# Kernel tuning notes

Hardware: AMD Instinct MI355X
Metric: run time of the kernel (lower is better)

The kernel has to match this reference:

```python
import jax, jax.numpy as jnp
import numpy as np

DIM = 1024
HIDDEN = 2816  # multiple_of * ceil(int(2*4096/3)/multiple_of)
N_MODALITIES = 2
B, S = 8, 4096


def setup_inputs() -> dict:
    key = jax.random.key(0)
    k_x, k_m, k1, k2, k3 = jax.random.split(key, 5)
    x = jax.random.normal(k_x, (B, S, DIM), dtype=jnp.float32)
    modality_ids = jax.random.randint(k_m, (B, S), 0, N_MODALITIES, dtype=jnp.int32)
    in_std = DIM ** -0.5
    out_std = HIDDEN ** -0.5
    # Linear weight layout: [out_features, in_features], stacked over modalities.
    W1 = jax.random.normal(k1, (N_MODALITIES, HIDDEN, DIM), dtype=jnp.float32) * in_std
    W3 = jax.random.normal(k3, (N_MODALITIES, HIDDEN, DIM), dtype=jnp.float32) * in_std
    W2 = jax.random.normal(k2, (N_MODALITIES, DIM, HIDDEN), dtype=jnp.float32) * out_std
    return {"x": x, "modality_ids": modality_ids, "W1": W1, "W2": W2, "W3": W3}


def reference(x, modality_ids, W1, W2, W3):
    # Masked per-modality SwiGLU; equivalent to gather -> expert MLP -> scatter.
    output = jnp.zeros_like(x)
    for m in range(N_MODALITIES):  # small fixed modality count
        mask = (modality_ids == m)[..., None]          # [B, S, 1]
        x1 = jnp.einsum('bsd,hd->bsh', x, W1[m])       # gate proj
        x3 = jnp.einsum('bsd,hd->bsh', x, W3[m])       # up proj
        out_m = jnp.einsum('bsh,dh->bsd', jax.nn.silu(x1) * x3, W2[m])
        output = output + jnp.where(mask, out_m, 0.0)
    return output
```

## Files before the change

kernel.cpp:

```cpp
#include <hip/hip_runtime.h>
#include <stdint.h>

#define DIMK 1024
#define HID  2816

typedef __attribute__((ext_vector_type(8))) __bf16 bf16x8;
typedef __attribute__((ext_vector_type(4))) float  f32x4;

typedef const __attribute__((address_space(1))) void* gas1_t;
typedef __attribute__((address_space(3))) void*       las3_t;

__device__ __forceinline__ uint16_t f2bf(float f) {
  uint32_t u = __float_as_uint(f);
  u += 0x7FFFu + ((u >> 16) & 1u);
  return (uint16_t)(u >> 16);
}

__device__ __forceinline__ void gload16(const uint16_t* g, uint16_t* l) {
  __builtin_amdgcn_global_load_lds((gas1_t)g, (las3_t)l, 16, 0, 0);
}

template<int N> __device__ __forceinline__ void wait_vm() {
  if constexpr (N == 0)      asm volatile("s_waitcnt vmcnt(0)" ::: "memory");
  else if constexpr (N == 2) asm volatile("s_waitcnt vmcnt(2)" ::: "memory");
  else                       asm volatile("s_waitcnt vmcnt(6)" ::: "memory");
}

__device__ __forceinline__ void stage_half(const uint16_t* g, long stride,
                                           uint16_t* lds, int wv, int lane) {
  const int rsub = lane >> 3;
  const int gsw  = ((lane & 7) ^ rsub) << 3;
#pragma unroll
  for (int j = 0; j < 2; ++j) {
    const int blk = j * 8 + wv;
    gload16(g + (long)(blk * 8 + rsub) * stride + gsw,
            lds + blk * 512 + lane * 8);
  }
}

__device__ __forceinline__ bf16x8 ldsf(const uint16_t* lds, int r, int g) {
  return *reinterpret_cast<const bf16x8*>(lds + r * 64 + ((g ^ (r & 7)) << 3));
}


__global__ void count_kernel(const int* __restrict__ mids, int* __restrict__ bc, int T) {
  const int b = blockIdx.x, t = threadIdx.x;
  const int token = b * 256 + t;
  const int lane = t & 63, wv = t >> 6;
  const int m = (token < T) ? mids[token] : -1;
  unsigned long long m0 = __ballot(m == 0);
  unsigned long long m1 = __ballot(m == 1);
  __shared__ int w0[4], w1[4];
  if (lane == 0) { w0[wv] = __popcll(m0); w1[wv] = __popcll(m1); }
  __syncthreads();
  if (t == 0) {
    bc[2 * b]     = w0[0] + w0[1] + w0[2] + w0[3];
    bc[2 * b + 1] = w1[0] + w1[1] + w1[2] + w1[3];
  }
}

__global__ void scan_kernel(const int* __restrict__ bc, int* __restrict__ base,
                            int* __restrict__ counters, int nb) {
  __shared__ int s0[256], s1[256];
  const int t = threadIdx.x;
  const int v0 = (t < nb) ? bc[2 * t] : 0;
  const int v1 = (t < nb) ? bc[2 * t + 1] : 0;
  s0[t] = v0; s1[t] = v1;
  __syncthreads();
  for (int off = 1; off < 256; off <<= 1) {
    int a0 = (t >= off) ? s0[t - off] : 0;
    int a1 = (t >= off) ? s1[t - off] : 0;
    __syncthreads();
    s0[t] += a0; s1[t] += a1;
    __syncthreads();
  }
  if (t < nb) { base[2 * t] = s0[t] - v0; base[2 * t + 1] = s1[t] - v1; }
  if (t == nb - 1) { counters[0] = s0[t]; counters[1] = s1[t]; }
}

__global__ void slot_kernel(const int* __restrict__ mids, const int* __restrict__ base,
                            const int* __restrict__ counters, int* __restrict__ tok,
                            int* __restrict__ slotof, int T) {
  const int b = blockIdx.x, t = threadIdx.x;
  const int token = b * 256 + t;
  const int lane = t & 63, wv = t >> 6;
  const int m = (token < T) ? mids[token] : -1;
  unsigned long long m0 = __ballot(m == 0);
  unsigned long long m1 = __ballot(m == 1);
  __shared__ int w0[4], w1[4];
  if (lane == 0) { w0[wv] = __popcll(m0); w1[wv] = __popcll(m1); }
  __syncthreads();
  int pre0 = 0, pre1 = 0;
  for (int w = 0; w < wv; ++w) { pre0 += w0[w]; pre1 += w1[w]; }
  if (token >= T) return;
  const unsigned long long below = (1ULL << lane) - 1ULL;
  const int c0 = counters[0];
  const int al0 = ((c0 + 255) >> 8) << 8;
  int slot;
  if (m == 0) slot = base[2 * b] + pre0 + __popcll(m0 & below);
  else        slot = al0 + base[2 * b + 1] + pre1 + __popcll(m1 & below);
  tok[slot] = token;
  slotof[token] = slot;
}

__global__ void copy_kernel(const float* __restrict__ x, const int* __restrict__ slotof,
                            uint16_t* __restrict__ xg, int T) {
  const int token = blockIdx.x * 4 + (threadIdx.x >> 6);
  if (token >= T) return;
  const int lane = threadIdx.x & 63;
  const int slot = slotof[token];
  const float4* src = (const float4*)(x + (long)token * DIMK);
  uint16_t* dst = xg + (long)slot * DIMK;
#pragma unroll
  for (int j = 0; j < 4; ++j) {
    float4 v = src[lane + 64 * j];
    ushort4 o;
    o.x = f2bf(v.x); o.y = f2bf(v.y); o.z = f2bf(v.z); o.w = f2bf(v.w);
    *(ushort4*)(dst + (lane + 64 * j) * 4) = o;
  }
}

__global__ void convert_kernel(const float* __restrict__ src, uint16_t* __restrict__ dst, long n) {
  long i = ((long)blockIdx.x * blockDim.x + threadIdx.x) * 4;
  if (i >= n) return;
  float4 v = *(const float4*)(src + i);
  ushort4 o;
  o.x = f2bf(v.x); o.y = f2bf(v.y); o.z = f2bf(v.z); o.w = f2bf(v.w);
  *(ushort4*)(dst + i) = o;
}


template<bool PF, int W0, int W2>
__device__ __forceinline__ void g1_tile(
    const uint16_t* Ac, const uint16_t* B1c, const uint16_t* B3c,
    uint16_t* An, uint16_t* B1n, uint16_t* B3n,
    const uint16_t* gA, const uint16_t* gB1, const uint16_t* gB3, long ko,
    int wv, int lane, int wr, int wc, int lrow, int grp,
    f32x4 (&accG)[8][2], f32x4 (&accU)[8][2]) {
  bf16x8 a[4][2], b1[2][2], b3[2][2];
  wait_vm<W0>();
  __builtin_amdgcn_s_barrier();
  asm volatile("" ::: "memory");
#pragma unroll
  for (int m = 0; m < 4; ++m)
    a[m][0] = ldsf(Ac, m * 32 + wr * 16 + lrow, grp);
#pragma unroll
  for (int n = 0; n < 2; ++n) {
    b1[n][0] = ldsf(B1c, wc * 32 + n * 16 + lrow, grp);
    b3[n][0] = ldsf(B3c, wc * 32 + n * 16 + lrow, grp);
  }
  if constexpr (PF) {
    stage_half(gA  + ko, DIMK, An,  wv, lane);
    stage_half(gB1 + ko, DIMK, B1n, wv, lane);
    stage_half(gB3 + ko, DIMK, B3n, wv, lane);
  }
  asm volatile("s_waitcnt lgkmcnt(0)" ::: "memory");
  __builtin_amdgcn_sched_barrier(0);
  __builtin_amdgcn_s_setprio(1);
#pragma unroll
  for (int m = 0; m < 4; ++m)
#pragma unroll
    for (int n = 0; n < 2; ++n) {
      accG[m][n] = __builtin_amdgcn_mfma_f32_16x16x32_bf16(a[m][0], b1[n][0], accG[m][n], 0, 0, 0);
      accU[m][n] = __builtin_amdgcn_mfma_f32_16x16x32_bf16(a[m][0], b3[n][0], accU[m][n], 0, 0, 0);
    }
  __builtin_amdgcn_s_setprio(0);
#pragma unroll
  for (int m = 0; m < 4; ++m)
    a[m][1] = ldsf(Ac, m * 32 + wr * 16 + lrow, 4 + grp);
#pragma unroll
  for (int n = 0; n < 2; ++n) {
    b1[n][1] = ldsf(B1c, wc * 32 + n * 16 + lrow, 4 + grp);
    b3[n][1] = ldsf(B3c, wc * 32 + n * 16 + lrow, 4 + grp);
  }
  asm volatile("s_waitcnt lgkmcnt(0)" ::: "memory");
  __builtin_amdgcn_sched_barrier(0);
  __builtin_amdgcn_s_setprio(1);
#pragma unroll
  for (int m = 0; m < 4; ++m)
#pragma unroll
    for (int n = 0; n < 2; ++n) {
      accG[m][n] = __builtin_amdgcn_mfma_f32_16x16x32_bf16(a[m][1], b1[n][1], accG[m][n], 0, 0, 0);
      accU[m][n] = __builtin_amdgcn_mfma_f32_16x16x32_bf16(a[m][1], b3[n][1], accU[m][n], 0, 0, 0);
    }
  __builtin_amdgcn_s_setprio(0);
  wait_vm<W2>();
  __builtin_amdgcn_s_barrier();
  asm volatile("" ::: "memory");
#pragma unroll
  for (int m = 0; m < 4; ++m)
    a[m][0] = ldsf(Ac, (m + 4) * 32 + wr * 16 + lrow, grp);
  if constexpr (PF) stage_half(gA + 128 * DIMK + ko, DIMK, An + 128 * 64, wv, lane);
  asm volatile("s_waitcnt lgkmcnt(0)" ::: "memory");
  __builtin_amdgcn_sched_barrier(0);
  __builtin_amdgcn_s_setprio(1);
#pragma unroll
  for (int m = 0; m < 4; ++m)
#pragma unroll
    for (int n = 0; n < 2; ++n) {
      accG[m + 4][n] = __builtin_amdgcn_mfma_f32_16x16x32_bf16(a[m][0], b1[n][0], accG[m + 4][n], 0, 0, 0);
      accU[m + 4][n] = __builtin_amdgcn_mfma_f32_16x16x32_bf16(a[m][0], b3[n][0], accU[m + 4][n], 0, 0, 0);
    }
  __builtin_amdgcn_s_setprio(0);
#pragma unroll
  for (int m = 0; m < 4; ++m)
    a[m][1] = ldsf(Ac, (m + 4) * 32 + wr * 16 + lrow, 4 + grp);
  asm volatile("s_waitcnt lgkmcnt(0)" ::: "memory");
  __builtin_amdgcn_sched_barrier(0);
  __builtin_amdgcn_s_setprio(1);
#pragma unroll
  for (int m = 0; m < 4; ++m)
#pragma unroll
    for (int n = 0; n < 2; ++n) {
      accG[m + 4][n] = __builtin_amdgcn_mfma_f32_16x16x32_bf16(a[m][1], b1[n][1], accG[m + 4][n], 0, 0, 0);
      accU[m + 4][n] = __builtin_amdgcn_mfma_f32_16x16x32_bf16(a[m][1], b3[n][1], accU[m + 4][n], 0, 0, 0);
    }
  __builtin_amdgcn_s_setprio(0);
}

__global__ __launch_bounds__(512, 2) void gemm1_kernel(
    const uint16_t* __restrict__ xg, const uint16_t* __restrict__ w1b,
    const uint16_t* __restrict__ w3b, uint16_t* __restrict__ hbuf,
    const int* __restrict__ counters) {
  __shared__ __align__(16) uint16_t lsA[2][256 * 64];
  __shared__ __align__(16) uint16_t lsB1[2][128 * 64];
  __shared__ __align__(16) uint16_t lsB3[2][128 * 64];

  const int c0 = counters[0], c1 = counters[1];
  const int t0 = (c0 + 255) >> 8, t1 = (c1 + 255) >> 8;
  const int NHT = gridDim.y;
  const int nwg = gridDim.x * NHT;
  const int orig = blockIdx.y * gridDim.x + blockIdx.x;
  const int q = nwg >> 3, r = nwg & 7;
  const int xcd = orig & 7, loc = orig >> 3;
  const int swz = (xcd < r ? xcd * (q + 1) : r * (q + 1) + (xcd - r) * q) + loc;
  const int rt = swz / NHT;
  const int ht = swz - rt * NHT;
  if (rt >= t0 + t1) return;
  const int mod = (rt < t0) ? 0 : 1;
  const long row0 = (long)rt * 256;

  const int tid = threadIdx.x, lane = tid & 63, wv = tid >> 6;
  const int wr = wv >> 2, wc = wv & 3;
  const int lrow = lane & 15, grp = lane >> 4;

  const uint16_t* gA  = xg  + row0 * DIMK;
  const uint16_t* gB1 = w1b + ((long)mod * HID + ht * 128) * DIMK;
  const uint16_t* gB3 = w3b + ((long)mod * HID + ht * 128) * DIMK;

  f32x4 accG[8][2], accU[8][2];
#pragma unroll
  for (int m = 0; m < 8; ++m)
#pragma unroll
    for (int n = 0; n < 2; ++n) {
      accG[m][n] = {0.f, 0.f, 0.f, 0.f};
      accU[m][n] = {0.f, 0.f, 0.f, 0.f};
    }

  stage_half(gA,              DIMK, &lsA[0][0],        wv, lane);
  stage_half(gB1,             DIMK, &lsB1[0][0],       wv, lane);
  stage_half(gB3,             DIMK, &lsB3[0][0],       wv, lane);
  stage_half(gA + 128 * DIMK, DIMK, &lsA[0][128 * 64], wv, lane);

  const int NT = DIMK / 64;
  int cur = 0;
  for (int t = 0; t < NT - 1; ++t) {
    g1_tile<true, 2, 6>(&lsA[cur][0], &lsB1[cur][0], &lsB3[cur][0],
                        &lsA[cur ^ 1][0], &lsB1[cur ^ 1][0], &lsB3[cur ^ 1][0],
                        gA, gB1, gB3, (long)(t + 1) * 64,
                        wv, lane, wr, wc, lrow, grp, accG, accU);
    cur ^= 1;
  }
  g1_tile<false, 2, 0>(&lsA[cur][0], &lsB1[cur][0], &lsB3[cur][0],
                       &lsA[cur ^ 1][0], &lsB1[cur ^ 1][0], &lsB3[cur ^ 1][0],
                       gA, gB1, gB3, 0,
                       wv, lane, wr, wc, lrow, grp, accG, accU);

#pragma unroll
  for (int m = 0; m < 8; ++m)
#pragma unroll
    for (int n = 0; n < 2; ++n) {
      const int col = ht * 128 + wc * 32 + n * 16 + lrow;
#pragma unroll
      for (int i = 0; i < 4; ++i) {
        const long row = row0 + m * 32 + wr * 16 + grp * 4 + i;
        float g = accG[m][n][i];
        float u = accU[m][n][i];
        float hv = (g / (1.f + __expf(-g))) * u;
        hbuf[row * HID + col] = f2bf(hv);
      }
    }
}


template<bool PF, int W0, int W2>
__device__ __forceinline__ void g2_tile(
    const uint16_t* Ac, const uint16_t* Bc, uint16_t* An, uint16_t* Bn,
    const uint16_t* gA, const uint16_t* gB, long ko,
    int wv, int lane, int wr, int wc, int lrow, int grp,
    f32x4 (&acc)[8][4]) {
  bf16x8 a[4][2], b[4][2];
  wait_vm<W0>();
  __builtin_amdgcn_s_barrier();
  asm volatile("" ::: "memory");
#pragma unroll
  for (int m = 0; m < 4; ++m)
    a[m][0] = ldsf(Ac, m * 32 + wr * 16 + lrow, grp);
#pragma unroll
  for (int n = 0; n < 4; ++n)
    b[n][0] = ldsf(Bc, wc * 64 + n * 16 + lrow, grp);
  if constexpr (PF) {
    stage_half(gA + ko,             HID, An,            wv, lane);
    stage_half(gB + ko,             HID, Bn,            wv, lane);
    stage_half(gB + 128 * HID + ko, HID, Bn + 128 * 64, wv, lane);
  }
  asm volatile("s_waitcnt lgkmcnt(0)" ::: "memory");
  __builtin_amdgcn_sched_barrier(0);
  __builtin_amdgcn_s_setprio(1);
#pragma unroll
  for (int m = 0; m < 4; ++m)
#pragma unroll
    for (int n = 0; n < 4; ++n)
      acc[m][n] = __builtin_amdgcn_mfma_f32_16x16x32_bf16(a[m][0], b[n][0], acc[m][n], 0, 0, 0);
  __builtin_amdgcn_s_setprio(0);
#pragma unroll
  for (int m = 0; m < 4; ++m)
    a[m][1] = ldsf(Ac, m * 32 + wr * 16 + lrow, 4 + grp);
#pragma unroll
  for (int n = 0; n < 4; ++n)
    b[n][1] = ldsf(Bc, wc * 64 + n * 16 + lrow, 4 + grp);
  asm volatile("s_waitcnt lgkmcnt(0)" ::: "memory");
  __builtin_amdgcn_sched_barrier(0);
  __builtin_amdgcn_s_setprio(1);
#pragma unroll
  for (int m = 0; m < 4; ++m)
#pragma unroll
    for (int n = 0; n < 4; ++n)
      acc[m][n] = __builtin_amdgcn_mfma_f32_16x16x32_bf16(a[m][1], b[n][1], acc[m][n], 0, 0, 0);
  __builtin_amdgcn_s_setprio(0);
  wait_vm<W2>();
  __builtin_amdgcn_s_barrier();
  asm volatile("" ::: "memory");
#pragma unroll
  for (int m = 0; m < 4; ++m)
    a[m][0] = ldsf(Ac, (m + 4) * 32 + wr * 16 + lrow, grp);
  if constexpr (PF) stage_half(gA + 128 * HID + ko, HID, An + 128 * 64, wv, lane);
  asm volatile("s_waitcnt lgkmcnt(0)" ::: "memory");
  __builtin_amdgcn_sched_barrier(0);
  __builtin_amdgcn_s_setprio(1);
#pragma unroll
  for (int m = 0; m < 4; ++m)
#pragma unroll
    for (int n = 0; n < 4; ++n)
      acc[m + 4][n] = __builtin_amdgcn_mfma_f32_16x16x32_bf16(a[m][0], b[n][0], acc[m + 4][n], 0, 0, 0);
  __builtin_amdgcn_s_setprio(0);
#pragma unroll
  for (int m = 0; m < 4; ++m)
    a[m][1] = ldsf(Ac, (m + 4) * 32 + wr * 16 + lrow, 4 + grp);
  asm volatile("s_waitcnt lgkmcnt(0)" ::: "memory");
  __builtin_amdgcn_sched_barrier(0);
  __builtin_amdgcn_s_setprio(1);
#pragma unroll
  for (int m = 0; m < 4; ++m)
#pragma unroll
    for (int n = 0; n < 4; ++n)
      acc[m + 4][n] = __builtin_amdgcn_mfma_f32_16x16x32_bf16(a[m][1], b[n][1], acc[m + 4][n], 0, 0, 0);
  __builtin_amdgcn_s_setprio(0);
}

__global__ __launch_bounds__(512, 2) void gemm2_kernel(
    const uint16_t* __restrict__ hbuf, const uint16_t* __restrict__ w2b,
    const int* __restrict__ counters, const int* __restrict__ tok,
    float* __restrict__ out) {
  __shared__ __align__(16) uint16_t lsA[2][256 * 64];
  __shared__ __align__(16) uint16_t lsB[2][256 * 64];

  const int c0 = counters[0], c1 = counters[1];
  const int t0 = (c0 + 255) >> 8, t1 = (c1 + 255) >> 8;
  const int NCT = gridDim.y;
  const int nwg = gridDim.x * NCT;
  const int orig = blockIdx.y * gridDim.x + blockIdx.x;
  const int q = nwg >> 3, r = nwg & 7;
  const int xcd = orig & 7, loc = orig >> 3;
  const int swz = (xcd < r ? xcd * (q + 1) : r * (q + 1) + (xcd - r) * q) + loc;
  const int rt = swz / NCT;
  const int ct = swz - rt * NCT;
  if (rt >= t0 + t1) return;
  const int mod = (rt < t0) ? 0 : 1;
  const long row0 = (long)rt * 256;
  const int vlimit = (mod == 0) ? c0 : t0 * 256 + c1;

  const int tid = threadIdx.x, lane = tid & 63, wv = tid >> 6;
  const int wr = wv >> 2, wc = wv & 3;
  const int lrow = lane & 15, grp = lane >> 4;

  const uint16_t* gA = hbuf + row0 * HID;
  const uint16_t* gB = w2b + ((long)mod * DIMK + ct * 256) * HID;

  f32x4 acc[8][4];
#pragma unroll
  for (int m = 0; m < 8; ++m)
#pragma unroll
    for (int n = 0; n < 4; ++n) acc[m][n] = {0.f, 0.f, 0.f, 0.f};

  stage_half(gA,             HID, &lsA[0][0],        wv, lane);
  stage_half(gB,             HID, &lsB[0][0],        wv, lane);
  stage_half(gB + 128 * HID, HID, &lsB[0][128 * 64], wv, lane);
  stage_half(gA + 128 * HID, HID, &lsA[0][128 * 64], wv, lane);

  const int NT = HID / 64;
  int cur = 0;
  for (int t = 0; t < NT - 1; ++t) {
    g2_tile<true, 2, 6>(&lsA[cur][0], &lsB[cur][0],
                        &lsA[cur ^ 1][0], &lsB[cur ^ 1][0],
                        gA, gB, (long)(t + 1) * 64,
                        wv, lane, wr, wc, lrow, grp, acc);
    cur ^= 1;
  }
  g2_tile<false, 2, 0>(&lsA[cur][0], &lsB[cur][0],
                       &lsA[cur ^ 1][0], &lsB[cur ^ 1][0],
                       gA, gB, 0,
                       wv, lane, wr, wc, lrow, grp, acc);

#pragma unroll
  for (int m = 0; m < 8; ++m)
#pragma unroll
    for (int n = 0; n < 4; ++n) {
      const int col = ct * 256 + wc * 64 + n * 16 + lrow;
#pragma unroll
      for (int i = 0; i < 4; ++i) {
        const int row = (int)row0 + m * 32 + wr * 16 + grp * 4 + i;
        if (row < vlimit) {
          out[(long)tok[row] * DIMK + col] = acc[m][n][i];
        }
      }
    }
}

extern "C" void kernel_launch(void* const* d_in, const int* in_sizes, int n_in,
                              void* d_out, int out_size, void* d_ws, size_t ws_size,
                              hipStream_t stream) {
  const float* x    = (const float*)d_in[0];
  const int*   mids = (const int*)d_in[1];
  const float* W1   = (const float*)d_in[2];
  const float* W2   = (const float*)d_in[3];
  const float* W3   = (const float*)d_in[4];
  float* out = (float*)d_out;

  const int T   = in_sizes[1];
  const int NB  = (T + 255) / 256;
  const int CAP = ((T + 255) & ~255) + 256;

  char* ws = (char*)d_ws;
  int* counters = (int*)ws;
  int* bc   = (int*)(ws + 256);
  int* base = (int*)(ws + 256 + 2048);
  int* tok  = (int*)(ws + 256 + 4096);
  int* slotof = tok + ((CAP + 63) & ~63);
  size_t off = 256 + 4096 + (size_t)((CAP + 63) & ~63) * 4 + (size_t)((T + 63) & ~63) * 4;
  off = (off + 255) & ~(size_t)255;
  uint16_t* xg  = (uint16_t*)(ws + off); off += (size_t)CAP * DIMK * 2;
  uint16_t* w1b = (uint16_t*)(ws + off); off += (size_t)2 * HID * DIMK * 2;
  uint16_t* w3b = (uint16_t*)(ws + off); off += (size_t)2 * HID * DIMK * 2;
  uint16_t* w2b = (uint16_t*)(ws + off); off += (size_t)2 * DIMK * HID * 2;
  uint16_t* hbuf = (uint16_t*)(ws + off); off += (size_t)CAP * HID * 2;
  (void)ws_size; (void)n_in; (void)out_size;

  count_kernel<<<NB, 256, 0, stream>>>(mids, bc, T);
  scan_kernel<<<1, 256, 0, stream>>>(bc, base, counters, NB);
  slot_kernel<<<NB, 256, 0, stream>>>(mids, base, counters, tok, slotof, T);
  copy_kernel<<<(T + 3) / 4, 256, 0, stream>>>(x, slotof, xg, T);

  const long NW = (long)2 * HID * DIMK;
  const int cblk = (int)((NW / 4 + 255) / 256);
  convert_kernel<<<cblk, 256, 0, stream>>>(W1, w1b, NW);
  convert_kernel<<<cblk, 256, 0, stream>>>(W3, w3b, NW);
  convert_kernel<<<cblk, 256, 0, stream>>>(W2, w2b, NW);

  const int rtiles = CAP / 256;
  gemm1_kernel<<<dim3(rtiles, HID / 128), 512, 0, stream>>>(xg, w1b, w3b, hbuf, counters);
  gemm2_kernel<<<dim3(rtiles, DIMK / 256), 512, 0, stream>>>(hbuf, w2b, counters, tok, out);
}
```

Before: 767.2 us.

## Restructure GEMM main loops into 8-phase ping-pong schedule with barrier-separated MFMA clusters

Both GEMM kernels are rewritten around a two-k-tile iteration with eight phases. Each phase issues one LDS fragment load batch and one global-to-LDS stage, then runs a 16-MFMA cluster between explicit barriers with raised priority, in the style of a ping-pong schedule. Launch bounds drop from 2 to 1 workgroup per CU, so the two waves per SIMD interleave under explicit barriers instead of relying on occupancy. This adds many barriers and a finer vmcnt/lgkmcnt wait discipline, and risks stalls or hazards if the wait counts are off.

```diff
diff --git a/kernel.cpp b/kernel.cpp
--- a/kernel.cpp
+++ b/kernel.cpp
@@ -22,8 +22,18 @@
 
 template<int N> __device__ __forceinline__ void wait_vm() {
   if constexpr (N == 0)      asm volatile("s_waitcnt vmcnt(0)" ::: "memory");
-  else if constexpr (N == 2) asm volatile("s_waitcnt vmcnt(2)" ::: "memory");
-  else                       asm volatile("s_waitcnt vmcnt(6)" ::: "memory");
+  else if constexpr (N == 6) asm volatile("s_waitcnt vmcnt(6)" ::: "memory");
+}
+
+__device__ __forceinline__ void ph_sync() {
+  __builtin_amdgcn_s_barrier();
+  asm volatile("s_waitcnt lgkmcnt(0)" ::: "memory");
+  __builtin_amdgcn_sched_barrier(0);
+  __builtin_amdgcn_s_setprio(1);
+}
+__device__ __forceinline__ void ph_end() {
+  __builtin_amdgcn_s_setprio(0);
+  __builtin_amdgcn_s_barrier();
 }
 
 __device__ __forceinline__ void stage_half(const uint16_t* g, long stride,
@@ -40,6 +50,30 @@
 
 __device__ __forceinline__ bf16x8 ldsf(const uint16_t* lds, int r, int g) {
   return *reinterpret_cast<const bf16x8*>(lds + r * 64 + ((g ^ (r & 7)) << 3));
+}
+
+template<int MO>
+__device__ __forceinline__ void mfma16_g1(f32x4 (&acc)[8][2], const bf16x8 (&af)[4][2],
+                                          const bf16x8 (&bf)[2][2]) {
+#pragma unroll
+  for (int ks = 0; ks < 2; ++ks)
+#pragma unroll
+    for (int m = 0; m < 4; ++m)
+#pragma unroll
+      for (int n = 0; n < 2; ++n)
+        acc[m + MO][n] = __builtin_amdgcn_mfma_f32_16x16x32_bf16(af[m][ks], bf[n][ks], acc[m + MO][n], 0, 0, 0);
+}
+
+template<int MO, int NO>
+__device__ __forceinline__ void mfma16_g2(f32x4 (&acc)[8][4], const bf16x8 (&af)[4][2],
+                                          const bf16x8 (&bf)[4][2]) {
+#pragma unroll
+  for (int ks = 0; ks < 2; ++ks)
+#pragma unroll
+    for (int m = 0; m < 4; ++m)
+#pragma unroll
+      for (int n = 0; n < 2; ++n)
+        acc[m + MO][n + NO] = __builtin_amdgcn_mfma_f32_16x16x32_bf16(af[m][ks], bf[n + NO][ks], acc[m + MO][n + NO], 0, 0, 0);
 }
 
 
@@ -130,95 +164,95 @@
 }
 
 
-template<bool PF, int W0, int W2>
-__device__ __forceinline__ void g1_tile(
-    const uint16_t* Ac, const uint16_t* B1c, const uint16_t* B3c,
-    uint16_t* An, uint16_t* B1n, uint16_t* B3n,
-    const uint16_t* gA, const uint16_t* gB1, const uint16_t* gB3, long ko,
+template<bool LAST>
+__device__ __forceinline__ void g1_iter(
+    uint16_t* A0, uint16_t* B10, uint16_t* B30,
+    uint16_t* A1, uint16_t* B11, uint16_t* B31,
+    const uint16_t* gA, const uint16_t* gB1, const uint16_t* gB3,
+    long ko1, long ko2, long ko3,
     int wv, int lane, int wr, int wc, int lrow, int grp,
     f32x4 (&accG)[8][2], f32x4 (&accU)[8][2]) {
   bf16x8 a[4][2], b1[2][2], b3[2][2];
-  wait_vm<W0>();
-  __builtin_amdgcn_s_barrier();
-  asm volatile("" ::: "memory");
-#pragma unroll
-  for (int m = 0; m < 4; ++m)
-    a[m][0] = ldsf(Ac, m * 32 + wr * 16 + lrow, grp);
+
+#pragma unroll
+  for (int m = 0; m < 4; ++m) {
+    a[m][0] = ldsf(A0, m * 32 + wr * 16 + lrow, grp);
+    a[m][1] = ldsf(A0, m * 32 + wr * 16 + lrow, 4 + grp);
+  }
 #pragma unroll
   for (int n = 0; n < 2; ++n) {
-    b1[n][0] = ldsf(B1c, wc * 32 + n * 16 + lrow, grp);
-    b3[n][0] = ldsf(B3c, wc * 32 + n * 16 + lrow, grp);
-  }
-  if constexpr (PF) {
-    stage_half(gA  + ko, DIMK, An,  wv, lane);
-    stage_half(gB1 + ko, DIMK, B1n, wv, lane);
-    stage_half(gB3 + ko, DIMK, B3n, wv, lane);
-  }
-  asm volatile("s_waitcnt lgkmcnt(0)" ::: "memory");
-  __builtin_amdgcn_sched_barrier(0);
-  __builtin_amdgcn_s_setprio(1);
-#pragma unroll
-  for (int m = 0; m < 4; ++m)
-#pragma unroll
-    for (int n = 0; n < 2; ++n) {
-      accG[m][n] = __builtin_amdgcn_mfma_f32_16x16x32_bf16(a[m][0], b1[n][0], accG[m][n], 0, 0, 0);
-      accU[m][n] = __builtin_amdgcn_mfma_f32_16x16x32_bf16(a[m][0], b3[n][0], accU[m][n], 0, 0, 0);
-    }
-  __builtin_amdgcn_s_setprio(0);
-#pragma unroll
-  for (int m = 0; m < 4; ++m)
-    a[m][1] = ldsf(Ac, m * 32 + wr * 16 + lrow, 4 + grp);
+    b1[n][0] = ldsf(B10, wc * 32 + n * 16 + lrow, grp);
+    b1[n][1] = ldsf(B10, wc * 32 + n * 16 + lrow, 4 + grp);
+  }
+  stage_half(gA + 128 * DIMK + ko1, DIMK, A1 + 128 * 64, wv, lane);
+  asm volatile("s_waitcnt lgkmcnt(8)" ::: "memory");
+  ph_sync();
+  mfma16_g1<0>(accG, a, b1);
+  ph_end();
 #pragma unroll
   for (int n = 0; n < 2; ++n) {
-    b1[n][1] = ldsf(B1c, wc * 32 + n * 16 + lrow, 4 + grp);
-    b3[n][1] = ldsf(B3c, wc * 32 + n * 16 + lrow, 4 + grp);
-  }
-  asm volatile("s_waitcnt lgkmcnt(0)" ::: "memory");
-  __builtin_amdgcn_sched_barrier(0);
-  __builtin_amdgcn_s_setprio(1);
-#pragma unroll
-  for (int m = 0; m < 4; ++m)
-#pragma unroll
-    for (int n = 0; n < 2; ++n) {
-      accG[m][n] = __builtin_amdgcn_mfma_f32_16x16x32_bf16(a[m][1], b1[n][1], accG[m][n], 0, 0, 0);
-      accU[m][n] = __builtin_amdgcn_mfma_f32_16x16x32_bf16(a[m][1], b3[n][1], accU[m][n], 0, 0, 0);
-    }
-  __builtin_amdgcn_s_setprio(0);
-  wait_vm<W2>();
-  __builtin_amdgcn_s_barrier();
-  asm volatile("" ::: "memory");
-#pragma unroll
-  for (int m = 0; m < 4; ++m)
-    a[m][0] = ldsf(Ac, (m + 4) * 32 + wr * 16 + lrow, grp);
-  if constexpr (PF) stage_half(gA + 128 * DIMK + ko, DIMK, An + 128 * 64, wv, lane);
-  asm volatile("s_waitcnt lgkmcnt(0)" ::: "memory");
-  __builtin_amdgcn_sched_barrier(0);
-  __builtin_amdgcn_s_setprio(1);
-#pragma unroll
-  for (int m = 0; m < 4; ++m)
-#pragma unroll
-    for (int n = 0; n < 2; ++n) {
-      accG[m + 4][n] = __builtin_amdgcn_mfma_f32_16x16x32_bf16(a[m][0], b1[n][0], accG[m + 4][n], 0, 0, 0);
-      accU[m + 4][n] = __builtin_amdgcn_mfma_f32_16x16x32_bf16(a[m][0], b3[n][0], accU[m + 4][n], 0, 0, 0);
-    }
-  __builtin_amdgcn_s_setprio(0);
-#pragma unroll
-  for (int m = 0; m < 4; ++m)
-    a[m][1] = ldsf(Ac, (m + 4) * 32 + wr * 16 + lrow, 4 + grp);
-  asm volatile("s_waitcnt lgkmcnt(0)" ::: "memory");
-  __builtin_amdgcn_sched_barrier(0);
-  __builtin_amdgcn_s_setprio(1);
-#pragma unroll
-  for (int m = 0; m < 4; ++m)
-#pragma unroll
-    for (int n = 0; n < 2; ++n) {
-      accG[m + 4][n] = __builtin_amdgcn_mfma_f32_16x16x32_bf16(a[m][1], b1[n][1], accG[m + 4][n], 0, 0, 0);
-      accU[m + 4][n] = __builtin_amdgcn_mfma_f32_16x16x32_bf16(a[m][1], b3[n][1], accU[m + 4][n], 0, 0, 0);
-    }
-  __builtin_amdgcn_s_setprio(0);
-}
-
-__global__ __launch_bounds__(512, 2) void gemm1_kernel(
+    b3[n][0] = ldsf(B30, wc * 32 + n * 16 + lrow, grp);
+    b3[n][1] = ldsf(B30, wc * 32 + n * 16 + lrow, 4 + grp);
+  }
+  if constexpr (!LAST) stage_half(gA + ko2, DIMK, A0, wv, lane);
+  ph_sync();
+  mfma16_g1<0>(accU, a, b3);
+  ph_end();
+#pragma unroll
+  for (int m = 0; m < 4; ++m) {
+    a[m][0] = ldsf(A0, (m + 4) * 32 + wr * 16 + lrow, grp);
+    a[m][1] = ldsf(A0, (m + 4) * 32 + wr * 16 + lrow, 4 + grp);
+  }
+  if constexpr (!LAST) stage_half(gB1 + ko2, DIMK, B10, wv, lane);
+  ph_sync();
+  mfma16_g1<4>(accG, a, b1);
+  ph_end();
+  if constexpr (!LAST) { stage_half(gB3 + ko2, DIMK, B30, wv, lane); wait_vm<6>(); }
+  else                 wait_vm<0>();
+  ph_sync();
+  mfma16_g1<4>(accU, a, b3);
+  ph_end();
+
+#pragma unroll
+  for (int m = 0; m < 4; ++m) {
+    a[m][0] = ldsf(A1, m * 32 + wr * 16 + lrow, grp);
+    a[m][1] = ldsf(A1, m * 32 + wr * 16 + lrow, 4 + grp);
+  }
+#pragma unroll
+  for (int n = 0; n < 2; ++n) {
+    b1[n][0] = ldsf(B11, wc * 32 + n * 16 + lrow, grp);
+    b1[n][1] = ldsf(B11, wc * 32 + n * 16 + lrow, 4 + grp);
+  }
+  if constexpr (!LAST) stage_half(gA + 128 * DIMK + ko2, DIMK, A0 + 128 * 64, wv, lane);
+  asm volatile("s_waitcnt lgkmcnt(8)" ::: "memory");
+  ph_sync();
+  mfma16_g1<0>(accG, a, b1);
+  ph_end();
+#pragma unroll
+  for (int n = 0; n < 2; ++n) {
+    b3[n][0] = ldsf(B31, wc * 32 + n * 16 + lrow, grp);
+    b3[n][1] = ldsf(B31, wc * 32 + n * 16 + lrow, 4 + grp);
+  }
+  if constexpr (!LAST) stage_half(gA + ko3, DIMK, A1, wv, lane);
+  ph_sync();
+  mfma16_g1<0>(accU, a, b3);
+  ph_end();
+#pragma unroll
+  for (int m = 0; m < 4; ++m) {
+    a[m][0] = ldsf(A1, (m + 4) * 32 + wr * 16 + lrow, grp);
+    a[m][1] = ldsf(A1, (m + 4) * 32 + wr * 16 + lrow, 4 + grp);
+  }
+  if constexpr (!LAST) stage_half(gB1 + ko3, DIMK, B11, wv, lane);
+  ph_sync();
+  mfma16_g1<4>(accG, a, b1);
+  ph_end();
+  if constexpr (!LAST) { stage_half(gB3 + ko3, DIMK, B31, wv, lane); wait_vm<6>(); }
+  ph_sync();
+  mfma16_g1<4>(accU, a, b3);
+  ph_end();
+}
+
+__global__ __launch_bounds__(512, 1) void gemm1_kernel(
     const uint16_t* __restrict__ xg, const uint16_t* __restrict__ w1b,
     const uint16_t* __restrict__ w3b, uint16_t* __restrict__ hbuf,
     const int* __restrict__ counters) {
@@ -257,24 +291,30 @@
       accU[m][n] = {0.f, 0.f, 0.f, 0.f};
     }
 
-  stage_half(gA,              DIMK, &lsA[0][0],        wv, lane);
-  stage_half(gB1,             DIMK, &lsB1[0][0],       wv, lane);
-  stage_half(gB3,             DIMK, &lsB3[0][0],       wv, lane);
-  stage_half(gA + 128 * DIMK, DIMK, &lsA[0][128 * 64], wv, lane);
-
-  const int NT = DIMK / 64;
-  int cur = 0;
-  for (int t = 0; t < NT - 1; ++t) {
-    g1_tile<true, 2, 6>(&lsA[cur][0], &lsB1[cur][0], &lsB3[cur][0],
-                        &lsA[cur ^ 1][0], &lsB1[cur ^ 1][0], &lsB3[cur ^ 1][0],
-                        gA, gB1, gB3, (long)(t + 1) * 64,
-                        wv, lane, wr, wc, lrow, grp, accG, accU);
-    cur ^= 1;
-  }
-  g1_tile<false, 2, 0>(&lsA[cur][0], &lsB1[cur][0], &lsB3[cur][0],
-                       &lsA[cur ^ 1][0], &lsB1[cur ^ 1][0], &lsB3[cur ^ 1][0],
-                       gA, gB1, gB3, 0,
-                       wv, lane, wr, wc, lrow, grp, accG, accU);
+  uint16_t* A0  = &lsA[0][0];  uint16_t* A1  = &lsA[1][0];
+  uint16_t* B10 = &lsB1[0][0]; uint16_t* B11 = &lsB1[1][0];
+  uint16_t* B30 = &lsB3[0][0]; uint16_t* B31 = &lsB3[1][0];
+
+  stage_half(gA,              DIMK, A0,           wv, lane);
+  stage_half(gB1,             DIMK, B10,          wv, lane);
+  stage_half(gB3,             DIMK, B30,          wv, lane);
+  stage_half(gA + 128 * DIMK, DIMK, A0 + 128 * 64, wv, lane);
+  stage_half(gA + 64,         DIMK, A1,           wv, lane);
+  stage_half(gB1 + 64,        DIMK, B11,          wv, lane);
+  stage_half(gB3 + 64,        DIMK, B31,          wv, lane);
+  wait_vm<6>();
+  __builtin_amdgcn_s_barrier();
+
+  const int NITER = DIMK / 128;
+  for (int it = 0; it < NITER - 1; ++it) {
+    const long t = 2 * it;
+    g1_iter<false>(A0, B10, B30, A1, B11, B31, gA, gB1, gB3,
+                   (t + 1) * 64, (t + 2) * 64, (t + 3) * 64,
+                   wv, lane, wr, wc, lrow, grp, accG, accU);
+  }
+  g1_iter<true>(A0, B10, B30, A1, B11, B31, gA, gB1, gB3,
+                (long)(DIMK / 64 - 1) * 64, 0, 0,
+                wv, lane, wr, wc, lrow, grp, accG, accU);
 
 #pragma unroll
   for (int m = 0; m < 8; ++m)
@@ -293,82 +333,84 @@
 }
 
 
-template<bool PF, int W0, int W2>
-__device__ __forceinline__ void g2_tile(
-    const uint16_t* Ac, const uint16_t* Bc, uint16_t* An, uint16_t* Bn,
-    const uint16_t* gA, const uint16_t* gB, long ko,
+template<bool LAST>
+__device__ __forceinline__ void g2_iter(
+    uint16_t* A0, uint16_t* B0, uint16_t* A1, uint16_t* B1b,
+    const uint16_t* gA, const uint16_t* gB,
+    long ko1, long ko2, long ko3,
     int wv, int lane, int wr, int wc, int lrow, int grp,
     f32x4 (&acc)[8][4]) {
   bf16x8 a[4][2], b[4][2];
-  wait_vm<W0>();
-  __builtin_amdgcn_s_barrier();
-  asm volatile("" ::: "memory");
-#pragma unroll
-  for (int m = 0; m < 4; ++m)
-    a[m][0] = ldsf(Ac, m * 32 + wr * 16 + lrow, grp);
-#pragma unroll
-  for (int n = 0; n < 4; ++n)
-    b[n][0] = ldsf(Bc, wc * 64 + n * 16 + lrow, grp);
-  if constexpr (PF) {
-    stage_half(gA + ko,             HID, An,            wv, lane);
-    stage_half(gB + ko,             HID, Bn,            wv, lane);
-    stage_half(gB + 128 * HID + ko, HID, Bn + 128 * 64, wv, lane);
-  }
-  asm volatile("s_waitcnt lgkmcnt(0)" ::: "memory");
-  __builtin_amdgcn_sched_barrier(0);
-  __builtin_amdgcn_s_setprio(1);
-#pragma unroll
-  for (int m = 0; m < 4; ++m)
-#pragma unroll
-    for (int n = 0; n < 4; ++n)
-      acc[m][n] = __builtin_amdgcn_mfma_f32_16x16x32_bf16(a[m][0], b[n][0], acc[m][n], 0, 0, 0);
-  __builtin_amdgcn_s_setprio(0);
-#pragma unroll
-  for (int m = 0; m < 4; ++m)
-    a[m][1] = ldsf(Ac, m * 32 + wr * 16 + lrow, 4 + grp);
-#pragma unroll
-  for (int n = 0; n < 4; ++n)
-    b[n][1] = ldsf(Bc, wc * 64 + n * 16 + lrow, 4 + grp);
-  asm volatile("s_waitcnt lgkmcnt(0)" ::: "memory");
-  __builtin_amdgcn_sched_barrier(0);
-  __builtin_amdgcn_s_setprio(1);
-#pragma unroll
-  for (int m = 0; m < 4; ++m)
-#pragma unroll
-    for (int n = 0; n < 4; ++n)
-      acc[m][n] = __builtin_amdgcn_mfma_f32_16x16x32_bf16(a[m][1], b[n][1], acc[m][n], 0, 0, 0);
-  __builtin_amdgcn_s_setprio(0);
-  wait_vm<W2>();
-  __builtin_amdgcn_s_barrier();
-  asm volatile("" ::: "memory");
-#pragma unroll
-  for (int m = 0; m < 4; ++m)
-    a[m][0] = ldsf(Ac, (m + 4) * 32 + wr * 16 + lrow, grp);
-  if constexpr (PF) stage_half(gA + 128 * HID + ko, HID, An + 128 * 64, wv, lane);
-  asm volatile("s_waitcnt lgkmcnt(0)" ::: "memory");
-  __builtin_amdgcn_sched_barrier(0);
-  __builtin_amdgcn_s_setprio(1);
-#pragma unroll
-  for (int m = 0; m < 4; ++m)
-#pragma unroll
-    for (int n = 0; n < 4; ++n)
-      acc[m + 4][n] = __builtin_amdgcn_mfma_f32_16x16x32_bf16(a[m][0], b[n][0], acc[m + 4][n], 0, 0, 0);
-  __builtin_amdgcn_s_setprio(0);
-#pragma unroll
-  for (int m = 0; m < 4; ++m)
-    a[m][1] = ldsf(Ac, (m + 4) * 32 + wr * 16 + lrow, 4 + grp);
-  asm volatile("s_waitcnt lgkmcnt(0)" ::: "memory");
-  __builtin_amdgcn_sched_barrier(0);
-  __builtin_amdgcn_s_setprio(1);
-#pragma unroll
-  for (int m = 0; m < 4; ++m)
-#pragma unroll
-    for (int n = 0; n < 4; ++n)
-      acc[m + 4][n] = __builtin_amdgcn_mfma_f32_16x16x32_bf16(a[m][1], b[n][1], acc[m + 4][n], 0, 0, 0);
-  __builtin_amdgcn_s_setprio(0);
-}
-
-__global__ __launch_bounds__(512, 2) void gemm2_kernel(
+
+#pragma unroll
+  for (int m = 0; m < 4; ++m) {
+    a[m][0] = ldsf(A0, m * 32 + wr * 16 + lrow, grp);
+    a[m][1] = ldsf(A0, m * 32 + wr * 16 + lrow, 4 + grp);
+  }
+#pragma unroll
+  for (int n = 0; n < 4; ++n) {
+    b[n][0] = ldsf(B0, wc * 64 + n * 16 + lrow, grp);
+    b[n][1] = ldsf(B0, wc * 64 + n * 16 + lrow, 4 + grp);
+  }
+  stage_half(gA + 128 * HID + ko1, HID, A1 + 128 * 64, wv, lane);
+  asm volatile("s_waitcnt lgkmcnt(8)" ::: "memory");
+  ph_sync();
+  mfma16_g2<0, 0>(acc, a, b);
+  ph_end();
+  if constexpr (!LAST) stage_half(gA + ko2, HID, A0, wv, lane);
+  ph_sync();
+  mfma16_g2<0, 2>(acc, a, b);
+  ph_end();
+#pragma unroll
+  for (int m = 0; m < 4; ++m) {
+    a[m][0] = ldsf(A0, (m + 4) * 32 + wr * 16 + lrow, grp);
+    a[m][1] = ldsf(A0, (m + 4) * 32 + wr * 16 + lrow, 4 + grp);
+  }
+  if constexpr (!LAST) stage_half(gB + ko2, HID, B0, wv, lane);
+  ph_sync();
+  mfma16_g2<4, 0>(acc, a, b);
+  ph_end();
+  if constexpr (!LAST) { stage_half(gB + 128 * HID + ko2, HID, B0 + 128 * 64, wv, lane); wait_vm<6>(); }
+  else                 wait_vm<0>();
+  ph_sync();
+  mfma16_g2<4, 2>(acc, a, b);
+  ph_end();
+
+#pragma unroll
+  for (int m = 0; m < 4; ++m) {
+    a[m][0] = ldsf(A1, m * 32 + wr * 16 + lrow, grp);
+    a[m][1] = ldsf(A1, m * 32 + wr * 16 + lrow, 4 + grp);
+  }
+#pragma unroll
+  for (int n = 0; n < 4; ++n) {
+    b[n][0] = ldsf(B1b, wc * 64 + n * 16 + lrow, grp);
+    b[n][1] = ldsf(B1b, wc * 64 + n * 16 + lrow, 4 + grp);
+  }
+  if constexpr (!LAST) stage_half(gA + 128 * HID + ko2, HID, A0 + 128 * 64, wv, lane);
+  asm volatile("s_waitcnt lgkmcnt(8)" ::: "memory");
+  ph_sync();
+  mfma16_g2<0, 0>(acc, a, b);
+  ph_end();
+  if constexpr (!LAST) stage_half(gA + ko3, HID, A1, wv, lane);
+  ph_sync();
+  mfma16_g2<0, 2>(acc, a, b);
+  ph_end();
+#pragma unroll
+  for (int m = 0; m < 4; ++m) {
+    a[m][0] = ldsf(A1, (m + 4) * 32 + wr * 16 + lrow, grp);
+    a[m][1] = ldsf(A1, (m + 4) * 32 + wr * 16 + lrow, 4 + grp);
+  }
+  if constexpr (!LAST) stage_half(gB + ko3, HID, B1b, wv, lane);
+  ph_sync();
+  mfma16_g2<4, 0>(acc, a, b);
+  ph_end();
+  if constexpr (!LAST) { stage_half(gB + 128 * HID + ko3, HID, B1b + 128 * 64, wv, lane); wait_vm<6>(); }
+  ph_sync();
+  mfma16_g2<4, 2>(acc, a, b);
+  ph_end();
+}
+
+__global__ __launch_bounds__(512, 1) void gemm2_kernel(
     const uint16_t* __restrict__ hbuf, const uint16_t* __restrict__ w2b,
     const int* __restrict__ counters, const int* __restrict__ tok,
     float* __restrict__ out) {
@@ -403,24 +445,29 @@
 #pragma unroll
     for (int n = 0; n < 4; ++n) acc[m][n] = {0.f, 0.f, 0.f, 0.f};
 
-  stage_half(gA,             HID, &lsA[0][0],        wv, lane);
-  stage_half(gB,             HID, &lsB[0][0],        wv, lane);
-  stage_half(gB + 128 * HID, HID, &lsB[0][128 * 64], wv, lane);
-  stage_half(gA + 128 * HID, HID, &lsA[0][128 * 64], wv, lane);
-
-  const int NT = HID / 64;
-  int cur = 0;
-  for (int t = 0; t < NT - 1; ++t) {
-    g2_tile<true, 2, 6>(&lsA[cur][0], &lsB[cur][0],
-                        &lsA[cur ^ 1][0], &lsB[cur ^ 1][0],
-                        gA, gB, (long)(t + 1) * 64,
-                        wv, lane, wr, wc, lrow, grp, acc);
-    cur ^= 1;
-  }
-  g2_tile<false, 2, 0>(&lsA[cur][0], &lsB[cur][0],
-                       &lsA[cur ^ 1][0], &lsB[cur ^ 1][0],
-                       gA, gB, 0,
-                       wv, lane, wr, wc, lrow, grp, acc);
+  uint16_t* A0  = &lsA[0][0]; uint16_t* A1  = &lsA[1][0];
+  uint16_t* B0  = &lsB[0][0]; uint16_t* B1b = &lsB[1][0];
+
+  stage_half(gA,                  HID, A0,            wv, lane);
+  stage_half(gB,                  HID, B0,            wv, lane);
+  stage_half(gB + 128 * HID,      HID, B0 + 128 * 64, wv, lane);
+  stage_half(gA + 128 * HID,      HID, A0 + 128 * 64, wv, lane);
+  stage_half(gA + 64,             HID, A1,            wv, lane);
+  stage_half(gB + 64,             HID, B1b,           wv, lane);
+  stage_half(gB + 128 * HID + 64, HID, B1b + 128 * 64, wv, lane);
+  wait_vm<6>();
+  __builtin_amdgcn_s_barrier();
+
+  const int NITER = HID / 128;
+  for (int it = 0; it < NITER - 1; ++it) {
+    const long t = 2 * it;
+    g2_iter<false>(A0, B0, A1, B1b, gA, gB,
+                   (t + 1) * 64, (t + 2) * 64, (t + 3) * 64,
+                   wv, lane, wr, wc, lrow, grp, acc);
+  }
+  g2_iter<true>(A0, B0, A1, B1b, gA, gB,
+                (long)(HID / 64 - 1) * 64, 0, 0,
+                wv, lane, wr, wc, lrow, grp, acc);
 
 #pragma unroll
   for (int m = 0; m < 8; ++m)
```

Result: slower. 791.7 us (+3.2%).
